# Performance work log

Hardware: AMD Instinct MI355X
Metric: run time of the kernel (lower is better)

## Reference

```python
import jax, jax.numpy as jnp
import numpy as np
from jax import lax

SIGMA = 1.0

def _rbf_kernel(x, sigma):
    # squared euclidean pairwise distances: ||xi||^2 + ||xj||^2 - 2 xi.xj  -> (n, n)
    sq = jnp.sum(x * x, axis=-1)
    d2 = sq[:, None] + sq[None, :] - 2.0 * (x @ x.T)
    d2 = jnp.maximum(d2, 0.0)
    return jnp.exp(-d2 / (2.0 * sigma * sigma))

def _center_kernel(K):
    # Mathematically identical to K - U@K - K@U + U@K@U with U = ones/n:
    # subtract column means, row means, add grand mean.
    col_mean = jnp.mean(K, axis=0, keepdims=True)   # (1, n) == U@K rows
    row_mean = jnp.mean(K, axis=1, keepdims=True)   # (n, 1) == K@U cols
    grand = jnp.mean(K)
    return K - col_mean - row_mean + grand

def _hsic_step(x, y, sigma):
    n = x.shape[0]
    Kx = _center_kernel(_rbf_kernel(x, sigma))
    Ky = _center_kernel(_rbf_kernel(y, sigma))
    # trace(Kx @ Ky) without materializing the product
    return jnp.einsum('ij,ji->', Kx, Ky) / float((n - 1) ** 2)

def setup_inputs() -> dict:
    key = jax.random.key(0)
    kx, ky = jax.random.split(key)
    N, D1, D2, L = 4096, 64, 64, 16
    X = jax.random.normal(kx, (N, D1, L), dtype=jnp.float32)
    Y = jax.random.normal(ky, (N, D2, L), dtype=jnp.float32)
    return {"X": X, "Y": Y}

def reference(X, Y):
    # X: (N, D1, L), Y: (N, D2, L); sum HSIC over timesteps L
    xs = jnp.moveaxis(X, -1, 0)  # (L, N, D1)
    ys = jnp.moveaxis(Y, -1, 0)  # (L, N, D2)

    def body(acc, xy):
        x, y = xy
        return acc + _hsic_step(x, y, SIGMA), None

    total, _ = lax.scan(body, jnp.float32(0.0), (xs, ys))
    return total
```

## Files before the change

### kernel.cpp

```cpp
#include <hip/hip_runtime.h>
#include <hip/hip_bf16.h>

typedef __attribute__((ext_vector_type(8))) short bf16x8;
typedef __attribute__((ext_vector_type(4))) float f32x4;

#define NN 4096
#define DD 64
#define LL 16
#define SCALE 1.2011224087864498f
#define THR -24.0f

__device__ __forceinline__ ushort f2bf(float f) {
    unsigned int u = __float_as_uint(f);
    unsigned int r = u + 0x7FFFu + ((u >> 16) & 1u);
    return (ushort)(r >> 16);
}
__device__ __forceinline__ float bf2f(ushort u) {
    return __uint_as_float(((unsigned int)u) << 16);
}

__device__ __forceinline__ void gload_lds16(const void* g, void* l) {
    __builtin_amdgcn_global_load_lds((const __attribute__((address_space(1))) unsigned int*)g,
                                     (__attribute__((address_space(3))) unsigned int*)l, 16, 0, 0);
}
__device__ __forceinline__ void gload_lds4(const void* g, void* l) {
    __builtin_amdgcn_global_load_lds((const __attribute__((address_space(1))) unsigned int*)g,
                                     (__attribute__((address_space(3))) unsigned int*)l, 4, 0, 0);
}

__global__ void prep_kernel(const float* __restrict__ X, const float* __restrict__ Y,
                            ushort* __restrict__ Xb, ushort* __restrict__ Yb,
                            float* __restrict__ hx, float* __restrict__ hy) {
    const float* in = blockIdx.y ? Y : X;
    ushort* outb    = blockIdx.y ? Yb : Xb;
    float* h        = blockIdx.y ? hy : hx;

    __shared__ float lds[64 * 17];
    __shared__ float psum[16][17];

    int n = blockIdx.x;
    int t = threadIdx.x;
    const float* row = in + (size_t)n * (DD * LL);

#pragma unroll
    for (int r = 0; r < 4; ++r) {
        int e = t + r * 256;
        lds[(e >> 4) * 17 + (e & 15)] = row[e];
    }
    __syncthreads();

    int l = t >> 4, c = t & 15;
    float p = 0.f;
    ushort4 w;
    {
        float v0 = lds[(c * 4 + 0) * 17 + l] * SCALE;
        float v1 = lds[(c * 4 + 1) * 17 + l] * SCALE;
        float v2 = lds[(c * 4 + 2) * 17 + l] * SCALE;
        float v3 = lds[(c * 4 + 3) * 17 + l] * SCALE;
        ushort u0 = f2bf(v0), u1 = f2bf(v1), u2 = f2bf(v2), u3 = f2bf(v3);
        float b0 = bf2f(u0), b1 = bf2f(u1), b2 = bf2f(u2), b3 = bf2f(u3);
        p = b0 * b0 + b1 * b1 + b2 * b2 + b3 * b3;
        w.x = u0; w.y = u1; w.z = u2; w.w = u3;
    }
    int cs = (c >> 1) ^ (n & 7);
    *reinterpret_cast<ushort4*>(outb + ((size_t)l * NN + n) * DD + cs * 8 + (c & 1) * 4) = w;

    psum[l][c] = p;
    __syncthreads();
    if (t < 16) {
        float s = 0.f;
#pragma unroll
        for (int i = 0; i < 16; ++i) s += psum[t][i];
        h[t * NN + n] = 0.5f * s;
    }
}

#define BUF_BYTES 8448
#define H_OFF 8192
#define NBUF 4

__device__ __forceinline__ void stage_tile(char* smem, int buf, int wave, int lane,
                                           const ushort* __restrict__ Xl, const ushort* __restrict__ Yl,
                                           const float* __restrict__ hxl, const float* __restrict__ hyl,
                                           int jb) {
    char* base = smem + buf * BUF_BYTES;
    const ushort* mat = (wave < 2) ? Xl : Yl;
#pragma unroll
    for (int q = 0; q < 2; ++q) {
        int ridx = wave * 2 + q;
        int rbase = (ridx & 3) * 8;
        const ushort* src = mat + (size_t)(jb + rbase + (lane >> 3)) * DD + (lane & 7) * 8;
        gload_lds16(src, base + ridx * 1024);
    }
    const float* hsrc = (lane < 32) ? (hxl + jb + lane) : (hyl + jb + (lane - 32));
    gload_lds4(hsrc, base + H_OFF);
}

__global__ __launch_bounds__(256, 2) void hsic_tri(
    const ushort* __restrict__ Xb, const ushort* __restrict__ Yb,
    const float* __restrict__ hx, const float* __restrict__ hy,
    float* __restrict__ a_raw, float* __restrict__ b_raw, float* __restrict__ t1) {

    int blk = blockIdx.x;
    int l = (blk & 7) * 2 + ((blk >> 3) & 1);
    int rest = blk >> 4;
    int p = rest >> 2;
    int seg = rest & 3;
    int c = 128 - 8 * p;
    int u0 = seg * 34, u1 = u0 + 34;

    int wave = threadIdx.x >> 6;
    int lane = threadIdx.x & 63;
    int lrow = lane & 15;
    int khi  = lane >> 4;

    const ushort* Xl = Xb + (size_t)l * (NN * DD);
    const ushort* Yl = Yb + (size_t)l * (NN * DD);
    const float* hxl = hx + l * NN;
    const float* hyl = hy + l * NN;

    __shared__ __align__(16) char smem[NBUF * BUF_BYTES];

    float t1_1 = 0.f, t1_2 = 0.f;

    int offb[2][2];
#pragma unroll
    for (int cg = 0; cg < 2; ++cg)
#pragma unroll
        for (int kc = 0; kc < 2; ++kc)
            offb[cg][kc] = (cg * 16 + lrow) * 128 + (((kc * 4 + khi) ^ (lrow & 7)) * 16);

    auto run_phase = [&](int ti, int jt0, int cnt) {
        __syncthreads();
        int ibase = ti * 256 + wave * 64;

        bf16x8 ax[4][2], ay[4][2];
        f32x4 nhxi4[4], nhyi4[4];
#pragma unroll
        for (int rg = 0; rg < 4; ++rg) {
            int arow = ibase + rg * 16 + lrow;
#pragma unroll
            for (int kc = 0; kc < 2; ++kc) {
                int cs = (kc * 4 + khi) ^ (arow & 7);
                ax[rg][kc] = *reinterpret_cast<const bf16x8*>(Xl + (size_t)arow * DD + cs * 8);
                ay[rg][kc] = *reinterpret_cast<const bf16x8*>(Yl + (size_t)arow * DD + cs * 8);
            }
            int crow = ibase + rg * 16 + khi * 4;
            f32x4 hv = *reinterpret_cast<const f32x4*>(hxl + crow);
            nhxi4[rg] = -hv;
            f32x4 hw = *reinterpret_cast<const f32x4*>(hyl + crow);
            nhyi4[rg] = -hw;
        }

        float rpx[4][4] = {}, rpy[4][4] = {};

        stage_tile(smem, 0, wave, lane, Xl, Yl, hxl, hyl, jt0 * 32);
        if (cnt > 1) stage_tile(smem, 1, wave, lane, Xl, Yl, hxl, hyl, (jt0 + 1) * 32);

        for (int k = 0; k < cnt; ++k) {
            if (k + 2 < cnt)
                stage_tile(smem, (k + 2) & (NBUF - 1), wave, lane, Xl, Yl, hxl, hyl, (jt0 + k + 2) * 32);

            if (k + 2 < cnt)      asm volatile("s_waitcnt vmcnt(6)" ::: "memory");
            else if (k + 1 < cnt) asm volatile("s_waitcnt vmcnt(3)" ::: "memory");
            else                  asm volatile("s_waitcnt vmcnt(0)" ::: "memory");
            __builtin_amdgcn_s_barrier();
            __builtin_amdgcn_sched_barrier(0);

            int jt = jt0 + k;
            int jb = jt * 32;
            bool band = (jt - 8 * ti) < 8;

            const char* bufc = smem + (k & (NBUF - 1)) * BUF_BYTES;
            const float* hbuf = (const float*)(bufc + H_OFF);

            float hxj[2], hyj[2];
#pragma unroll
            for (int cg = 0; cg < 2; ++cg) {
                hxj[cg] = hbuf[cg * 16 + lrow];
                hyj[cg] = hbuf[32 + cg * 16 + lrow];
            }

            bf16x8 bfx[2][2], bfy[2][2];
#pragma unroll
            for (int cg = 0; cg < 2; ++cg)
#pragma unroll
                for (int kc = 0; kc < 2; ++kc) {
                    bfx[cg][kc] = *reinterpret_cast<const bf16x8*>(bufc + offb[cg][kc]);
                    bfy[cg][kc] = *reinterpret_cast<const bf16x8*>(bufc + 4096 + offb[cg][kc]);
                }

            f32x4 gx[4][2], gy[4][2];
#pragma unroll
            for (int rg = 0; rg < 4; ++rg)
#pragma unroll
                for (int cg = 0; cg < 2; ++cg) {
                    gx[rg][cg] = nhxi4[rg] - hxj[cg];
                    gy[rg][cg] = nhyi4[rg] - hyj[cg];
                }

#pragma unroll
            for (int rg = 0; rg < 4; ++rg)
#pragma unroll
                for (int cg = 0; cg < 2; ++cg)
#pragma unroll
                    for (int kc = 0; kc < 2; ++kc) {
                        gx[rg][cg] = __builtin_amdgcn_mfma_f32_16x16x32_bf16(ax[rg][kc], bfx[cg][kc], gx[rg][cg], 0, 0, 0);
                        gy[rg][cg] = __builtin_amdgcn_mfma_f32_16x16x32_bf16(ay[rg][kc], bfy[cg][kc], gy[rg][cg], 0, 0, 0);
                    }

            float mt[16];
#pragma unroll
            for (int rg = 0; rg < 4; ++rg)
#pragma unroll
                for (int cg = 0; cg < 2; ++cg) {
                    int idx = rg * 2 + cg;
                    mt[idx]     = fmaxf(fmaxf(fmaxf(gx[rg][cg][0], gx[rg][cg][1]), gx[rg][cg][2]), gx[rg][cg][3]);
                    mt[8 + idx] = fmaxf(fmaxf(fmaxf(gy[rg][cg][0], gy[rg][cg][1]), gy[rg][cg][2]), gy[rg][cg][3]);
                }
            float m0 = fmaxf(fmaxf(fmaxf(mt[0], mt[1]), mt[2]), mt[3]);
            float m1 = fmaxf(fmaxf(fmaxf(mt[4], mt[5]), mt[6]), mt[7]);
            float m2 = fmaxf(fmaxf(fmaxf(mt[8], mt[9]), mt[10]), mt[11]);
            float m3 = fmaxf(fmaxf(fmaxf(mt[12], mt[13]), mt[14]), mt[15]);
            float mall = fmaxf(fmaxf(m0, m1), fmaxf(m2, m3));

            if (__ballot(mall >= THR)) {
                float cax[2] = {0.f, 0.f}, cay[2] = {0.f, 0.f};
#pragma unroll
                for (int rg = 0; rg < 4; ++rg)
#pragma unroll
                    for (int cg = 0; cg < 2; ++cg)
#pragma unroll
                        for (int q = 0; q < 4; ++q) {
                            float kxv = __builtin_exp2f(gx[rg][cg][q]);
                            float kyv = __builtin_exp2f(gy[rg][cg][q]);
                            rpx[rg][q] += kxv;
                            rpy[rg][q] += kyv;
                            float prod = kxv * kyv;
                            if (band) {
                                t1_1 += prod;
                            } else {
                                t1_2 += prod;
                                cax[cg] += kxv;
                                cay[cg] += kyv;
                            }
                        }
                if (!band) {
#pragma unroll
                    for (int cg = 0; cg < 2; ++cg) {
                        float vx = cax[cg], vy = cay[cg];
                        vx += __shfl_xor(vx, 16); vx += __shfl_xor(vx, 32);
                        vy += __shfl_xor(vy, 16); vy += __shfl_xor(vy, 32);
                        if (khi == 0) {
                            atomicAdd(&a_raw[l * NN + jb + cg * 16 + lrow], vx);
                            atomicAdd(&b_raw[l * NN + jb + cg * 16 + lrow], vy);
                        }
                    }
                }
            }
        }

#pragma unroll
        for (int rg = 0; rg < 4; ++rg)
#pragma unroll
            for (int q = 0; q < 4; ++q) {
                float vx = rpx[rg][q], vy = rpy[rg][q];
#pragma unroll
                for (int sh = 1; sh < 16; sh <<= 1) {
                    vx += __shfl_xor(vx, sh);
                    vy += __shfl_xor(vy, sh);
                }
                if (lrow == 0) {
                    int row = ibase + rg * 16 + khi * 4 + q;
                    atomicAdd(&a_raw[l * NN + row], vx);
                    atomicAdd(&b_raw[l * NN + row], vy);
                }
            }
    };

    int a_lo = u0, a_hi = (u1 < c) ? u1 : c;
    if (a_lo < a_hi) run_phase(p, 8 * p + a_lo, a_hi - a_lo);

    int b_lo = (u0 > c) ? u0 : c, b_hi = u1;
    if (b_lo < b_hi) run_phase(15 - p, 8 * (15 - p) + (b_lo - c), b_hi - b_lo);

    float v = t1_1 + 2.f * t1_2;
#pragma unroll
    for (int sh = 1; sh < 64; sh <<= 1) v += __shfl_xor(v, sh);
    if (lane == 0) atomicAdd(&t1[l], v);
}

__global__ void finalize_kernel(const float* __restrict__ a_raw, const float* __restrict__ b_raw,
                                const float* __restrict__ t1, float* __restrict__ out) {
    int l = blockIdx.x;
    int t = threadIdx.x;
    int lane = t & 63, w = t >> 6;

    float sab = 0.f, sa = 0.f, sb = 0.f;
    for (int i = t; i < NN; i += 256) {
        float av = a_raw[l * NN + i], bv = b_raw[l * NN + i];
        sab = __builtin_fmaf(av, bv, sab);
        sa += av;
        sb += bv;
    }
#pragma unroll
    for (int s = 1; s < 64; s <<= 1) {
        sab += __shfl_xor(sab, s);
        sa  += __shfl_xor(sa, s);
        sb  += __shfl_xor(sb, s);
    }
    __shared__ float sh[3][4];
    if (lane == 0) { sh[0][w] = sab; sh[1][w] = sa; sh[2][w] = sb; }
    __syncthreads();
    if (t == 0) {
        float rab = sh[0][0] + sh[0][1] + sh[0][2] + sh[0][3];
        float ra  = sh[1][0] + sh[1][1] + sh[1][2] + sh[1][3];
        float rb  = sh[2][0] + sh[2][1] + sh[2][2] + sh[2][3];
        const float n = (float)NN;
        float S = t1[l] - (2.f / n) * rab + (ra * rb) / (n * n);
        atomicAdd(out, S / (4095.f * 4095.f));
    }
}

extern "C" void kernel_launch(void* const* d_in, const int* in_sizes, int n_in,
                              void* d_out, int out_size, void* d_ws, size_t ws_size,
                              hipStream_t stream) {
    const float* X = (const float*)d_in[0];
    const float* Y = (const float*)d_in[1];
    float* out = (float*)d_out;
    char* ws = (char*)d_ws;

    const size_t XB_OFF  = 0;
    const size_t YB_OFF  = 8388608;
    const size_t HX_OFF  = 16777216;
    const size_t HY_OFF  = 17039360;
    const size_t A_OFF   = 17301504;
    const size_t B_OFF   = 17563648;
    const size_t T1_OFF  = 17825792;

    ushort* Xb  = (ushort*)(ws + XB_OFF);
    ushort* Yb  = (ushort*)(ws + YB_OFF);
    float* hx   = (float*)(ws + HX_OFF);
    float* hy   = (float*)(ws + HY_OFF);
    float* a_raw = (float*)(ws + A_OFF);
    float* b_raw = (float*)(ws + B_OFF);
    float* t1    = (float*)(ws + T1_OFF);

    hipMemsetAsync(ws + A_OFF, 0, 2 * 262144 + 64, stream);
    hipMemsetAsync(d_out, 0, sizeof(float), stream);

    prep_kernel<<<dim3(NN, 2), 256, 0, stream>>>(X, Y, Xb, Yb, hx, hy);
    hsic_tri<<<512, 256, 0, stream>>>(Xb, Yb, hx, hy, a_raw, b_raw, t1);
    finalize_kernel<<<LL, 256, 0, stream>>>(a_raw, b_raw, t1, out);
}
```

Before: 87.54 us.

## Double-buffer LDS fragment reads, split work over more blocks, defer norm bias to exp

Doubles the grid to 1024 blocks with half-length column segments so more blocks share the work. The tile loop now reads the next tile's LDS fragments into a second register set while the current tile's MFMAs run, and stages three tiles ahead. The norm bias is no longer the MFMA accumulator init: MFMAs start from zero, a per-row threshold (built from the minimum row norm) decides skipping, and the bias is applied inside the exp. Row-sum accumulators are dropped in favour of per-tile shuffles and atomics, which cuts register pressure but adds many atomics on active tiles.

```diff
diff --git a/kernel.cpp b/kernel.cpp
--- a/kernel.cpp
+++ b/kernel.cpp
@@ -9,6 +9,10 @@
 #define LL 16
 #define SCALE 1.2011224087864498f
 #define THR -24.0f
+
+#define BUF_BYTES 8448
+#define H_OFF 8192
+#define NBUF 4
 
 __device__ __forceinline__ ushort f2bf(float f) {
     unsigned int u = __float_as_uint(f);
@@ -75,27 +79,6 @@
     }
 }
 
-#define BUF_BYTES 8448
-#define H_OFF 8192
-#define NBUF 4
-
-__device__ __forceinline__ void stage_tile(char* smem, int buf, int wave, int lane,
-                                           const ushort* __restrict__ Xl, const ushort* __restrict__ Yl,
-                                           const float* __restrict__ hxl, const float* __restrict__ hyl,
-                                           int jb) {
-    char* base = smem + buf * BUF_BYTES;
-    const ushort* mat = (wave < 2) ? Xl : Yl;
-#pragma unroll
-    for (int q = 0; q < 2; ++q) {
-        int ridx = wave * 2 + q;
-        int rbase = (ridx & 3) * 8;
-        const ushort* src = mat + (size_t)(jb + rbase + (lane >> 3)) * DD + (lane & 7) * 8;
-        gload_lds16(src, base + ridx * 1024);
-    }
-    const float* hsrc = (lane < 32) ? (hxl + jb + lane) : (hyl + jb + (lane - 32));
-    gload_lds4(hsrc, base + H_OFF);
-}
-
 __global__ __launch_bounds__(256, 2) void hsic_tri(
     const ushort* __restrict__ Xb, const ushort* __restrict__ Yb,
     const float* __restrict__ hx, const float* __restrict__ hy,
@@ -103,11 +86,10 @@
 
     int blk = blockIdx.x;
     int l = (blk & 7) * 2 + ((blk >> 3) & 1);
-    int rest = blk >> 4;
-    int p = rest >> 2;
-    int seg = rest & 3;
+    int p = (blk >> 4) & 7;
+    int seg = blk >> 7;
     int c = 128 - 8 * p;
-    int u0 = seg * 34, u1 = u0 + 34;
+    int u0 = seg * 17, u1 = u0 + 17;
 
     int wave = threadIdx.x >> 6;
     int lane = threadIdx.x & 63;
@@ -122,6 +104,7 @@
     __shared__ __align__(16) char smem[NBUF * BUF_BYTES];
 
     float t1_1 = 0.f, t1_2 = 0.f;
+    const f32x4 fzero = {0.f, 0.f, 0.f, 0.f};
 
     int offb[2][2];
 #pragma unroll
@@ -135,7 +118,8 @@
         int ibase = ti * 256 + wave * 64;
 
         bf16x8 ax[4][2], ay[4][2];
-        f32x4 nhxi4[4], nhyi4[4];
+        float thr2x[4], thr2y[4];
+        int crow[4];
 #pragma unroll
         for (int rg = 0; rg < 4; ++rg) {
             int arow = ibase + rg * 16 + lrow;
@@ -145,110 +129,116 @@
                 ax[rg][kc] = *reinterpret_cast<const bf16x8*>(Xl + (size_t)arow * DD + cs * 8);
                 ay[rg][kc] = *reinterpret_cast<const bf16x8*>(Yl + (size_t)arow * DD + cs * 8);
             }
-            int crow = ibase + rg * 16 + khi * 4;
-            f32x4 hv = *reinterpret_cast<const f32x4*>(hxl + crow);
-            nhxi4[rg] = -hv;
-            f32x4 hw = *reinterpret_cast<const f32x4*>(hyl + crow);
-            nhyi4[rg] = -hw;
+            crow[rg] = ibase + rg * 16 + khi * 4;
+            f32x4 hv = *reinterpret_cast<const f32x4*>(hxl + crow[rg]);
+            thr2x[rg] = THR + fminf(fminf(hv[0], hv[1]), fminf(hv[2], hv[3]));
+            f32x4 hw = *reinterpret_cast<const f32x4*>(hyl + crow[rg]);
+            thr2y[rg] = THR + fminf(fminf(hw[0], hw[1]), fminf(hw[2], hw[3]));
         }
 
-        float rpx[4][4] = {}, rpy[4][4] = {};
-
-        stage_tile(smem, 0, wave, lane, Xl, Yl, hxl, hyl, jt0 * 32);
-        if (cnt > 1) stage_tile(smem, 1, wave, lane, Xl, Yl, hxl, hyl, (jt0 + 1) * 32);
-
-        for (int k = 0; k < cnt; ++k) {
-            if (k + 2 < cnt)
-                stage_tile(smem, (k + 2) & (NBUF - 1), wave, lane, Xl, Yl, hxl, hyl, (jt0 + k + 2) * 32);
-
-            if (k + 2 < cnt)      asm volatile("s_waitcnt vmcnt(6)" ::: "memory");
-            else if (k + 1 < cnt) asm volatile("s_waitcnt vmcnt(3)" ::: "memory");
-            else                  asm volatile("s_waitcnt vmcnt(0)" ::: "memory");
-            __builtin_amdgcn_s_barrier();
-            __builtin_amdgcn_sched_barrier(0);
-
-            int jt = jt0 + k;
-            int jb = jt * 32;
-            bool band = (jt - 8 * ti) < 8;
-
-            const char* bufc = smem + (k & (NBUF - 1)) * BUF_BYTES;
-            const float* hbuf = (const float*)(bufc + H_OFF);
-
-            float hxj[2], hyj[2];
+        const ushort* sp = ((wave < 2) ? Xl : Yl)
+                         + (size_t)(jt0 * 32 + ((wave * 2) & 3) * 8 + (lane >> 3)) * DD
+                         + (lane & 7) * 8;
+        const float* sph = (lane < 32) ? (hxl + jt0 * 32 + lane) : (hyl + jt0 * 32 + (lane - 32));
+        int dst0 = (wave * 2) * 1024;
+        int sb = 0;
+
+        auto do_stage = [&]() {
+            char* base = smem + (sb & 3) * BUF_BYTES;
+            gload_lds16(sp, base + dst0);
+            gload_lds16(sp + 8 * DD, base + dst0 + 1024);
+            gload_lds4(sph, base + H_OFF);
+            sp += 32 * DD; sph += 32; ++sb;
+        };
+
+        int nst = cnt < 3 ? cnt : 3;
+        for (int s = 0; s < nst; ++s) do_stage();
+        if (nst == 3)      asm volatile("s_waitcnt vmcnt(6)" ::: "memory");
+        else if (nst == 2) asm volatile("s_waitcnt vmcnt(3)" ::: "memory");
+        else               asm volatile("s_waitcnt vmcnt(0)" ::: "memory");
+        __builtin_amdgcn_s_barrier();
+
+        bf16x8 bxA[2][2], byA[2][2], bxB[2][2], byB[2][2];
+        float hxjA[2], hyjA[2], hxjB[2], hyjB[2];
+        int bo = 0;
+
+        auto read_set = [&](bf16x8 (&bx)[2][2], bf16x8 (&by)[2][2],
+                            float (&hxj)[2], float (&hyj)[2]) {
+            const char* bc = smem + bo;
 #pragma unroll
             for (int cg = 0; cg < 2; ++cg) {
-                hxj[cg] = hbuf[cg * 16 + lrow];
-                hyj[cg] = hbuf[32 + cg * 16 + lrow];
-            }
-
-            bf16x8 bfx[2][2], bfy[2][2];
-#pragma unroll
-            for (int cg = 0; cg < 2; ++cg)
 #pragma unroll
                 for (int kc = 0; kc < 2; ++kc) {
-                    bfx[cg][kc] = *reinterpret_cast<const bf16x8*>(bufc + offb[cg][kc]);
-                    bfy[cg][kc] = *reinterpret_cast<const bf16x8*>(bufc + 4096 + offb[cg][kc]);
-                }
-
+                    bx[cg][kc] = *reinterpret_cast<const bf16x8*>(bc + offb[cg][kc]);
+                    by[cg][kc] = *reinterpret_cast<const bf16x8*>(bc + 4096 + offb[cg][kc]);
+                }
+                hxj[cg] = *reinterpret_cast<const float*>(bc + H_OFF + (cg * 16 + lrow) * 4);
+                hyj[cg] = *reinterpret_cast<const float*>(bc + H_OFF + 128 + (cg * 16 + lrow) * 4);
+            }
+            bo = (bo == (NBUF - 1) * BUF_BYTES) ? 0 : bo + BUF_BYTES;
+        };
+
+        auto compute = [&](bf16x8 (&bx)[2][2], bf16x8 (&by)[2][2],
+                           float (&hxj)[2], float (&hyj)[2], int jt) {
             f32x4 gx[4][2], gy[4][2];
+            __builtin_amdgcn_s_setprio(1);
 #pragma unroll
             for (int rg = 0; rg < 4; ++rg)
 #pragma unroll
                 for (int cg = 0; cg < 2; ++cg) {
-                    gx[rg][cg] = nhxi4[rg] - hxj[cg];
-                    gy[rg][cg] = nhyi4[rg] - hyj[cg];
-                }
-
+                    f32x4 t0 = __builtin_amdgcn_mfma_f32_16x16x32_bf16(ax[rg][0], bx[cg][0], fzero, 0, 0, 0);
+                    gx[rg][cg] = __builtin_amdgcn_mfma_f32_16x16x32_bf16(ax[rg][1], bx[cg][1], t0, 0, 0, 0);
+                    f32x4 t1v = __builtin_amdgcn_mfma_f32_16x16x32_bf16(ay[rg][0], by[cg][0], fzero, 0, 0, 0);
+                    gy[rg][cg] = __builtin_amdgcn_mfma_f32_16x16x32_bf16(ay[rg][1], by[cg][1], t1v, 0, 0, 0);
+                }
+            __builtin_amdgcn_s_setprio(0);
+
+            float dm = -1e30f;
 #pragma unroll
             for (int rg = 0; rg < 4; ++rg)
 #pragma unroll
-                for (int cg = 0; cg < 2; ++cg)
-#pragma unroll
-                    for (int kc = 0; kc < 2; ++kc) {
-                        gx[rg][cg] = __builtin_amdgcn_mfma_f32_16x16x32_bf16(ax[rg][kc], bfx[cg][kc], gx[rg][cg], 0, 0, 0);
-                        gy[rg][cg] = __builtin_amdgcn_mfma_f32_16x16x32_bf16(ay[rg][kc], bfy[cg][kc], gy[rg][cg], 0, 0, 0);
+                for (int cg = 0; cg < 2; ++cg) {
+                    float mx = fmaxf(fmaxf(gx[rg][cg][0], gx[rg][cg][1]), fmaxf(gx[rg][cg][2], gx[rg][cg][3]));
+                    float my = fmaxf(fmaxf(gy[rg][cg][0], gy[rg][cg][1]), fmaxf(gy[rg][cg][2], gy[rg][cg][3]));
+                    dm = fmaxf(dm, mx - (thr2x[rg] + hxj[cg]));
+                    dm = fmaxf(dm, my - (thr2y[rg] + hyj[cg]));
+                }
+
+            if (__ballot(dm >= 0.f)) {
+                bool band = (jt - 8 * ti) < 8;
+                int jb = jt * 32;
+                f32x4 hvx[4], hvy[4];
+#pragma unroll
+                for (int rg = 0; rg < 4; ++rg) {
+                    hvx[rg] = *reinterpret_cast<const f32x4*>(hxl + crow[rg]);
+                    hvy[rg] = *reinterpret_cast<const f32x4*>(hyl + crow[rg]);
+                }
+                float colx[2] = {0.f, 0.f}, coly[2] = {0.f, 0.f};
+#pragma unroll
+                for (int rg = 0; rg < 4; ++rg)
+#pragma unroll
+                    for (int q = 0; q < 4; ++q) {
+                        float kx0 = __builtin_exp2f(gx[rg][0][q] - hvx[rg][q] - hxj[0]);
+                        float kx1 = __builtin_exp2f(gx[rg][1][q] - hvx[rg][q] - hxj[1]);
+                        float ky0 = __builtin_exp2f(gy[rg][0][q] - hvy[rg][q] - hyj[0]);
+                        float ky1 = __builtin_exp2f(gy[rg][1][q] - hvy[rg][q] - hyj[1]);
+                        float pr = kx0 * ky0 + kx1 * ky1;
+                        if (band) t1_1 += pr; else t1_2 += pr;
+                        if (!band) { colx[0] += kx0; colx[1] += kx1; coly[0] += ky0; coly[1] += ky1; }
+                        float rx = kx0 + kx1, ry = ky0 + ky1;
+                        rx += __shfl_xor(rx, 1); rx += __shfl_xor(rx, 2);
+                        rx += __shfl_xor(rx, 4); rx += __shfl_xor(rx, 8);
+                        ry += __shfl_xor(ry, 1); ry += __shfl_xor(ry, 2);
+                        ry += __shfl_xor(ry, 4); ry += __shfl_xor(ry, 8);
+                        if (lrow == 0) {
+                            atomicAdd(&a_raw[l * NN + crow[rg] + q], rx);
+                            atomicAdd(&b_raw[l * NN + crow[rg] + q], ry);
+                        }
                     }
-
-            float mt[16];
-#pragma unroll
-            for (int rg = 0; rg < 4; ++rg)
-#pragma unroll
-                for (int cg = 0; cg < 2; ++cg) {
-                    int idx = rg * 2 + cg;
-                    mt[idx]     = fmaxf(fmaxf(fmaxf(gx[rg][cg][0], gx[rg][cg][1]), gx[rg][cg][2]), gx[rg][cg][3]);
-                    mt[8 + idx] = fmaxf(fmaxf(fmaxf(gy[rg][cg][0], gy[rg][cg][1]), gy[rg][cg][2]), gy[rg][cg][3]);
-                }
-            float m0 = fmaxf(fmaxf(fmaxf(mt[0], mt[1]), mt[2]), mt[3]);
-            float m1 = fmaxf(fmaxf(fmaxf(mt[4], mt[5]), mt[6]), mt[7]);
-            float m2 = fmaxf(fmaxf(fmaxf(mt[8], mt[9]), mt[10]), mt[11]);
-            float m3 = fmaxf(fmaxf(fmaxf(mt[12], mt[13]), mt[14]), mt[15]);
-            float mall = fmaxf(fmaxf(m0, m1), fmaxf(m2, m3));
-
-            if (__ballot(mall >= THR)) {
-                float cax[2] = {0.f, 0.f}, cay[2] = {0.f, 0.f};
-#pragma unroll
-                for (int rg = 0; rg < 4; ++rg)
-#pragma unroll
-                    for (int cg = 0; cg < 2; ++cg)
-#pragma unroll
-                        for (int q = 0; q < 4; ++q) {
-                            float kxv = __builtin_exp2f(gx[rg][cg][q]);
-                            float kyv = __builtin_exp2f(gy[rg][cg][q]);
-                            rpx[rg][q] += kxv;
-                            rpy[rg][q] += kyv;
-                            float prod = kxv * kyv;
-                            if (band) {
-                                t1_1 += prod;
-                            } else {
-                                t1_2 += prod;
-                                cax[cg] += kxv;
-                                cay[cg] += kyv;
-                            }
-                        }
                 if (!band) {
 #pragma unroll
                     for (int cg = 0; cg < 2; ++cg) {
-                        float vx = cax[cg], vy = cay[cg];
+                        float vx = colx[cg], vy = coly[cg];
                         vx += __shfl_xor(vx, 16); vx += __shfl_xor(vx, 32);
                         vy += __shfl_xor(vy, 16); vy += __shfl_xor(vy, 32);
                         if (khi == 0) {
@@ -258,24 +248,44 @@
                     }
                 }
             }
+        };
+
+        read_set(bxA, byA, hxjA, hyjA);
+
+        auto iter_head = [&](int m) {
+            if (m + 2 <= cnt - 1) asm volatile("s_waitcnt vmcnt(3)" ::: "memory");
+            else                  asm volatile("s_waitcnt vmcnt(0)" ::: "memory");
+            __builtin_amdgcn_s_barrier();
+            if (m + 3 <= cnt - 1) do_stage();
+        };
+
+        int m = 0;
+        while (true) {
+            if (m == cnt - 1) {
+                asm volatile("s_waitcnt lgkmcnt(0)" ::: "memory");
+                __builtin_amdgcn_sched_barrier(0);
+                compute(bxA, byA, hxjA, hyjA, jt0 + m);
+                break;
+            }
+            iter_head(m);
+            read_set(bxB, byB, hxjB, hyjB);
+            asm volatile("s_waitcnt lgkmcnt(10)" ::: "memory");
+            __builtin_amdgcn_sched_barrier(0);
+            compute(bxA, byA, hxjA, hyjA, jt0 + m);
+            ++m;
+            if (m == cnt - 1) {
+                asm volatile("s_waitcnt lgkmcnt(0)" ::: "memory");
+                __builtin_amdgcn_sched_barrier(0);
+                compute(bxB, byB, hxjB, hyjB, jt0 + m);
+                break;
+            }
+            iter_head(m);
+            read_set(bxA, byA, hxjA, hyjA);
+            asm volatile("s_waitcnt lgkmcnt(10)" ::: "memory");
+            __builtin_amdgcn_sched_barrier(0);
+            compute(bxB, byB, hxjB, hyjB, jt0 + m);
+            ++m;
         }
-
-#pragma unroll
-        for (int rg = 0; rg < 4; ++rg)
-#pragma unroll
-            for (int q = 0; q < 4; ++q) {
-                float vx = rpx[rg][q], vy = rpy[rg][q];
-#pragma unroll
-                for (int sh = 1; sh < 16; sh <<= 1) {
-                    vx += __shfl_xor(vx, sh);
-                    vy += __shfl_xor(vy, sh);
-                }
-                if (lrow == 0) {
-                    int row = ibase + rg * 16 + khi * 4 + q;
-                    atomicAdd(&a_raw[l * NN + row], vx);
-                    atomicAdd(&b_raw[l * NN + row], vy);
-                }
-            }
     };
 
     int a_lo = u0, a_hi = (u1 < c) ? u1 : c;
@@ -350,6 +360,6 @@
     hipMemsetAsync(d_out, 0, sizeof(float), stream);
 
     prep_kernel<<<dim3(NN, 2), 256, 0, stream>>>(X, Y, Xb, Yb, hx, hy);
-    hsic_tri<<<512, 256, 0, stream>>>(Xb, Yb, hx, hy, a_raw, b_raw, t1);
+    hsic_tri<<<1024, 256, 0, stream>>>(Xb, Yb, hx, hy, a_raw, b_raw, t1);
     finalize_kernel<<<LL, 256, 0, stream>>>(a_raw, b_raw, t1, out);
 }
```

New measurement: 195.8 us. 2.24x slower.

## Make each wave stage its own double-buffered tile to drop block barriers

Applied to the files above, without the earlier changes.

Each wave now loads the full 32-row X/Y tile plus norms into a private double buffer instead of the block cooperatively filling a shared 4-deep ring. This removes the per-iteration s_barrier and the phase-start __syncthreads, so waves run independently. Global/LDS traffic per block rises fourfold (each wave loads redundant data) and the prefetch depth drops from 2 to 1. s_setprio is also raised around the MFMA block to favour matrix issue.

```diff
diff --git a/kernel.cpp b/kernel.cpp
--- a/kernel.cpp
+++ b/kernel.cpp
@@ -77,21 +77,20 @@
 
 #define BUF_BYTES 8448
 #define H_OFF 8192
-#define NBUF 4
-
-__device__ __forceinline__ void stage_tile(char* smem, int buf, int wave, int lane,
+
+__device__ __forceinline__ void stage_wave(char* wbase, int buf, int lane,
                                            const ushort* __restrict__ Xl, const ushort* __restrict__ Yl,
                                            const float* __restrict__ hxl, const float* __restrict__ hyl,
                                            int jb) {
-    char* base = smem + buf * BUF_BYTES;
-    const ushort* mat = (wave < 2) ? Xl : Yl;
-#pragma unroll
-    for (int q = 0; q < 2; ++q) {
-        int ridx = wave * 2 + q;
-        int rbase = (ridx & 3) * 8;
-        const ushort* src = mat + (size_t)(jb + rbase + (lane >> 3)) * DD + (lane & 7) * 8;
-        gload_lds16(src, base + ridx * 1024);
-    }
+    char* base = wbase + buf * BUF_BYTES;
+    int row = lane >> 3;
+    int col = (lane & 7) * 8;
+#pragma unroll
+    for (int q = 0; q < 4; ++q)
+        gload_lds16(Xl + (size_t)(jb + q * 8 + row) * DD + col, base + q * 1024);
+#pragma unroll
+    for (int q = 0; q < 4; ++q)
+        gload_lds16(Yl + (size_t)(jb + q * 8 + row) * DD + col, base + 4096 + q * 1024);
     const float* hsrc = (lane < 32) ? (hxl + jb + lane) : (hyl + jb + (lane - 32));
     gload_lds4(hsrc, base + H_OFF);
 }
@@ -119,7 +118,8 @@
     const float* hxl = hx + l * NN;
     const float* hyl = hy + l * NN;
 
-    __shared__ __align__(16) char smem[NBUF * BUF_BYTES];
+    __shared__ __align__(16) char smem[4 * 2 * BUF_BYTES];
+    char* wbase = smem + wave * (2 * BUF_BYTES);
 
     float t1_1 = 0.f, t1_2 = 0.f;
 
@@ -131,7 +131,6 @@
             offb[cg][kc] = (cg * 16 + lrow) * 128 + (((kc * 4 + khi) ^ (lrow & 7)) * 16);
 
     auto run_phase = [&](int ti, int jt0, int cnt) {
-        __syncthreads();
         int ibase = ti * 256 + wave * 64;
 
         bf16x8 ax[4][2], ay[4][2];
@@ -154,24 +153,22 @@
 
         float rpx[4][4] = {}, rpy[4][4] = {};
 
-        stage_tile(smem, 0, wave, lane, Xl, Yl, hxl, hyl, jt0 * 32);
-        if (cnt > 1) stage_tile(smem, 1, wave, lane, Xl, Yl, hxl, hyl, (jt0 + 1) * 32);
+        stage_wave(wbase, 0, lane, Xl, Yl, hxl, hyl, jt0 * 32);
 
         for (int k = 0; k < cnt; ++k) {
-            if (k + 2 < cnt)
-                stage_tile(smem, (k + 2) & (NBUF - 1), wave, lane, Xl, Yl, hxl, hyl, (jt0 + k + 2) * 32);
-
-            if (k + 2 < cnt)      asm volatile("s_waitcnt vmcnt(6)" ::: "memory");
-            else if (k + 1 < cnt) asm volatile("s_waitcnt vmcnt(3)" ::: "memory");
-            else                  asm volatile("s_waitcnt vmcnt(0)" ::: "memory");
-            __builtin_amdgcn_s_barrier();
+            if (k + 1 < cnt) {
+                stage_wave(wbase, (k + 1) & 1, lane, Xl, Yl, hxl, hyl, (jt0 + k + 1) * 32);
+                asm volatile("s_waitcnt vmcnt(9)" ::: "memory");
+            } else {
+                asm volatile("s_waitcnt vmcnt(0)" ::: "memory");
+            }
             __builtin_amdgcn_sched_barrier(0);
 
             int jt = jt0 + k;
             int jb = jt * 32;
             bool band = (jt - 8 * ti) < 8;
 
-            const char* bufc = smem + (k & (NBUF - 1)) * BUF_BYTES;
+            const char* bufc = wbase + (k & 1) * BUF_BYTES;
             const float* hbuf = (const float*)(bufc + H_OFF);
 
             float hxj[2], hyj[2];
@@ -199,6 +196,7 @@
                     gy[rg][cg] = nhyi4[rg] - hyj[cg];
                 }
 
+            __builtin_amdgcn_s_setprio(1);
 #pragma unroll
             for (int rg = 0; rg < 4; ++rg)
 #pragma unroll
@@ -208,6 +206,7 @@
                         gx[rg][cg] = __builtin_amdgcn_mfma_f32_16x16x32_bf16(ax[rg][kc], bfx[cg][kc], gx[rg][cg], 0, 0, 0);
                         gy[rg][cg] = __builtin_amdgcn_mfma_f32_16x16x32_bf16(ay[rg][kc], bfy[cg][kc], gy[rg][cg], 0, 0, 0);
                     }
+            __builtin_amdgcn_s_setprio(0);
 
             float mt[16];
 #pragma unroll
```

Result: slower. 106.1 us (median of 2 runs) (+21.2%).
